# Optimization experiments

Hardware: AMD Instinct MI355X
Metric: run time of the kernel (lower is better)

The kernel has to match this reference:

```python
import jax, jax.numpy as jnp
import numpy as np
from jax import lax

FILTERS = [(1, 32), (2, 32), (3, 64), (4, 128), (5, 256), (6, 512), (7, 1024)]
CHAR_VOCAB, CHAR_DIM, MAX_CHARS = 262, 16, 50
N_FILTERS = sum(n for _, n in FILTERS)  # 2048
PROJ_DIM = 512
B, S = 16, 256


def setup_inputs() -> dict:
    key = jax.random.key(0)
    ks = jax.random.split(key, 32)
    inp = {}
    inp["words"] = jax.random.randint(ks[0], (B, S), 0, 50000)
    inp["chars"] = jax.random.randint(ks[1], (B, S, MAX_CHARS), 0, CHAR_VOCAB)
    inp["char_emb"] = jax.random.normal(ks[2], (CHAR_VOCAB, CHAR_DIM), jnp.float32) * 0.1
    for i, (w, n) in enumerate(FILTERS):
        inp[f"conv_w_{i}"] = jax.random.normal(ks[3 + i], (n, CHAR_DIM, w), jnp.float32) * 0.1
        inp[f"conv_b_{i}"] = jnp.zeros((n,), jnp.float32)
    for j in range(2):
        inp[f"hw_w_{j}"] = jax.random.normal(ks[12 + j], (2 * N_FILTERS, N_FILTERS), jnp.float32) * 0.02
        # Highway init: transform bias = 0, gate bias = 1
        inp[f"hw_b_{j}"] = jnp.concatenate([jnp.zeros((N_FILTERS,), jnp.float32), jnp.ones((N_FILTERS,), jnp.float32)])
    inp["proj_w"] = jax.random.normal(ks[20], (PROJ_DIM, N_FILTERS), jnp.float32) * 0.02
    inp["proj_b"] = jnp.zeros((PROJ_DIM,), jnp.float32)
    return inp


def _char_cnn(chars, char_emb, conv_ws, conv_bs, hw_ws, hw_bs, proj_w, proj_b):
    b, s, L = chars.shape
    # (B*S, CHAR_DIM, L)
    x = char_emb[chars].reshape(b * s, L, -1).transpose(0, 2, 1)
    convs = []
    for w, bias in zip(conv_ws, conv_bs):
        # Conv1d valid, NCW layout; y: (N, num, L-width+1)
        y = lax.conv_general_dilated(x, w, (1,), "VALID", dimension_numbers=("NCH", "OIH", "NCH"))
        y = y + bias[None, :, None]
        y = jnp.max(y, axis=-1)          # max over time
        convs.append(jax.nn.relu(y))      # activation
    h = jnp.concatenate(convs, axis=-1)   # (N, 2048)
    d = h.shape[-1]
    for W, bb in zip(hw_ws, hw_bs):
        p = h @ W.T + bb
        nonlinear = jax.nn.relu(p[:, :d])
        gate = jax.nn.sigmoid(p[:, d:])
        h = gate * h + (1.0 - gate) * nonlinear
    out = h @ proj_w.T + proj_b
    return out.reshape(b, s, -1)


def reference(words, chars, char_emb,
              conv_w_0, conv_b_0, conv_w_1, conv_b_1, conv_w_2, conv_b_2,
              conv_w_3, conv_b_3, conv_w_4, conv_b_4, conv_w_5, conv_b_5,
              conv_w_6, conv_b_6, hw_w_0, hw_b_0, hw_w_1, hw_b_1, proj_w, proj_b):
    conv_ws = [conv_w_0, conv_w_1, conv_w_2, conv_w_3, conv_w_4, conv_w_5, conv_w_6]
    conv_bs = [conv_b_0, conv_b_1, conv_b_2, conv_b_3, conv_b_4, conv_b_5, conv_b_6]
    return _char_cnn(chars, char_emb, conv_ws, conv_bs, [hw_w_0, hw_w_1], [hw_b_0, hw_b_1], proj_w, proj_b)
```

## Files before the change

### kernel.cpp

```cpp
#include <hip/hip_runtime.h>
#include <hip/hip_bf16.h>


#define NTOK 4096
#define NF   2048
#define KDIM 2048
#define HID  4096
#define PDIM 512

typedef __attribute__((ext_vector_type(4))) float floatx4;
typedef __attribute__((ext_vector_type(8))) short shortx8;

__device__ inline void async_copy16(const void* g, void* l) {
  __builtin_amdgcn_global_load_lds(
      (const __attribute__((address_space(1))) void*)(uintptr_t)g,
      (__attribute__((address_space(3))) void*)(uint32_t)(uintptr_t)l,
      16, 0, 0);
}

__global__ __launch_bounds__(256) void cvt_kernel(
    const float* __restrict__ s, __hip_bfloat16* __restrict__ d, int n) {
  int i = blockIdx.x * 256 + threadIdx.x;
  if (i < n) d[i] = __float2bfloat16(s[i]);
}

__global__ __launch_bounds__(256) void cvt_hw(
    const float* __restrict__ s, __hip_bfloat16* __restrict__ d) {
  int i = blockIdx.x * 256 + threadIdx.x;
  int r = i >> 11, k = i & 2047;
  int sr = (r >> 1) + (r & 1) * 2048;
  d[i] = __float2bfloat16(s[(size_t)sr * 2048 + k]);
}

__global__ __launch_bounds__(256) void conv_wprep(
    const float* __restrict__ w0, const float* __restrict__ w1,
    const float* __restrict__ w2, const float* __restrict__ w3,
    const float* __restrict__ w4, const float* __restrict__ w5,
    const float* __restrict__ w6,
    const float* __restrict__ b0, const float* __restrict__ b1,
    const float* __restrict__ b2, const float* __restrict__ b3,
    const float* __restrict__ b4, const float* __restrict__ b5,
    const float* __restrict__ b6, const float* __restrict__ emb,
    __hip_bfloat16* __restrict__ Wb, float* __restrict__ Bc,
    __hip_bfloat16* __restrict__ embb) {
  int idx = blockIdx.x * 256 + threadIdx.x;
  const int start[7] = {0, 32, 64, 128, 256, 512, 1024};
  const float* ws[7] = {w0, w1, w2, w3, w4, w5, w6};
  const float* bs[7] = {b0, b1, b2, b3, b4, b5, b6};
  if (idx < 262144) {
    int ch = idx >> 7, kp = idx & 127;
    int f = (ch >= 32) + (ch >= 64) + (ch >= 128) + (ch >= 256) +
            (ch >= 512) + (ch >= 1024);
    int w = f + 1, lc = ch - start[f];
    int d = kp & 15, k = kp >> 4;
    float v = (k < w) ? ws[f][((size_t)lc * 16 + d) * w + k] : 0.f;
    Wb[idx] = __float2bfloat16(v);
  } else if (idx < 262144 + 2048) {
    int ch = idx - 262144;
    int f = (ch >= 32) + (ch >= 64) + (ch >= 128) + (ch >= 256) +
            (ch >= 512) + (ch >= 1024);
    Bc[ch] = bs[f][ch - start[f]];
  } else if (idx < 262144 + 2048 + 4192) {
    int e = idx - 262144 - 2048;
    embb[e] = __float2bfloat16(emb[e]);
  }
}

template <int NKT, int NT, int ROWS>
__global__ __launch_bounds__(256) void conv_k(
    const int* __restrict__ chars, const __hip_bfloat16* __restrict__ embb,
    const __hip_bfloat16* __restrict__ Wb, const float* __restrict__ bias,
    __hip_bfloat16* __restrict__ h, int chbase) {
  __shared__ __align__(16) __hip_bfloat16 Xs[2 * 4 * ROWS * 24];
  int tid = threadIdx.x, wave = tid >> 6, lane = tid & 63;
  int frow = lane & 15, q = lane >> 4;
  int chb = chbase + blockIdx.y * 64;
  int tokbase = blockIdx.x * 32;

  shortx8 wreg[NKT][4];
#pragma unroll
  for (int kt = 0; kt < NKT; ++kt)
#pragma unroll
    for (int j = 0; j < 4; ++j)
      wreg[kt][j] = *(const shortx8*)(
          Wb + (size_t)(chb + j * 16 + frow) * 128 + kt * 32 + q * 8);

  float blane = bias[chb + lane];
  int Tvj[4];
#pragma unroll
  for (int j = 0; j < 4; ++j) {
    int ch = chb + j * 16 + frow;
    int w = 1 + (ch >= 32) + (ch >= 64) + (ch >= 128) + (ch >= 256) +
            (ch >= 512) + (ch >= 1024);
    Tvj[j] = 51 - w;
  }

  auto stage = [&](int g, int buf) {
    constexpr int NST = 4 * ROWS;
#pragma unroll
    for (int rep = 0; rep < (NST + 255) / 256; ++rep) {
      int rr = tid + rep * 256;
      if (rr < NST) {
        int tk = rr / ROWS, r = rr - tk * ROWS;
        __hip_bfloat16* dst = Xs + ((size_t)(buf * 4 + tk) * ROWS + r) * 24;
        if (r < 50) {
          int c = chars[(size_t)(tokbase + g * 4 + tk) * 50 + r];
          const shortx8* e = (const shortx8*)(embb + c * 16);
          *(shortx8*)(dst) = e[0];
          *(shortx8*)(dst + 8) = e[1];
        } else if (g <= 1) {
          shortx8 z = {0, 0, 0, 0, 0, 0, 0, 0};
          *(shortx8*)(dst) = z;
          *(shortx8*)(dst + 8) = z;
        }
      }
    }
  };

  stage(0, 0);
  __syncthreads();

  const floatx4 zero = {0.f, 0.f, 0.f, 0.f};
#pragma unroll 1
  for (int g = 0; g < 8; ++g) {
    if (g < 7) stage(g + 1, (g + 1) & 1);

    const __hip_bfloat16* Xw = Xs + (size_t)((g & 1) * 4 + wave) * ROWS * 24;
    floatx4 acc[NT][4];

#pragma unroll
    for (int kt = 0; kt < NKT; ++kt) {
      int kk = kt * 2 + (q >> 1);
      int d0 = (q & 1) * 8;
      shortx8 xf[NT];
#pragma unroll
      for (int i = 0; i < NT; ++i)
        xf[i] = *(const shortx8*)(Xw + (i * 16 + frow + kk) * 24 + d0);
#pragma unroll
      for (int i = 0; i < NT; ++i)
#pragma unroll
        for (int j = 0; j < 4; ++j) {
          if (kt == 0)
            acc[i][j] = __builtin_amdgcn_mfma_f32_16x16x32_bf16(
                xf[i], wreg[0][j], zero, 0, 0, 0);
          else
            acc[i][j] = __builtin_amdgcn_mfma_f32_16x16x32_bf16(
                xf[i], wreg[kt][j], acc[i][j], 0, 0, 0);
        }
    }

    float vj[4];
#pragma unroll
    for (int j = 0; j < 4; ++j) {
      float v = -1e30f;
#pragma unroll
      for (int i = 0; i < NT; ++i) {
#pragma unroll
        for (int r = 0; r < 4; ++r) {
          if (i < 2) {
            v = fmaxf(v, acc[i][j][r]);
          } else {
            int t = i * 16 + q * 4 + r;
            if (t < Tvj[j]) v = fmaxf(v, acc[i][j][r]);
          }
        }
      }
      v = fmaxf(v, __shfl_xor(v, 16));
      v = fmaxf(v, __shfl_xor(v, 32));
      vj[j] = v;
    }
    float r0 = (q & 2) ? vj[2] : vj[0];
    float r1 = (q & 2) ? vj[3] : vj[1];
    float rv = (q & 1) ? r1 : r0;
    int tok = tokbase + g * 4 + wave;
    h[(size_t)tok * NF + chb + lane] =
        __float2bfloat16(fmaxf(rv + blane, 0.f));
    __syncthreads();
  }
}

__global__ __launch_bounds__(256) void gemm_hw(
    const __hip_bfloat16* __restrict__ A, const __hip_bfloat16* __restrict__ B,
    const float* __restrict__ hwb, __hip_bfloat16* __restrict__ Hdst) {
  const int K = KDIM;
  __shared__ __align__(16) __hip_bfloat16 As[128 * 64];
  __shared__ __align__(16) __hip_bfloat16 Bs[128 * 64];
  int tid = threadIdx.x;
  int wave = tid >> 6, lane = tid & 63;
  int wr = wave >> 1, wc = wave & 1;
  int bn = blockIdx.y, bm = blockIdx.x;

  int sr8 = lane >> 3;
  int sc8 = lane & 7;
  int frow = lane & 15;
  int q    = lane >> 4;

  floatx4 acc[4][4];
  floatx4 zero = {0.f, 0.f, 0.f, 0.f};
#pragma unroll
  for (int i = 0; i < 4; ++i)
#pragma unroll
    for (int j = 0; j < 4; ++j) acc[i][j] = zero;

  const __hip_bfloat16* Ab = A + (size_t)bn * 128 * K;
  const __hip_bfloat16* Bb = B + (size_t)bm * 128 * K;

  for (int kb = 0; kb < K; kb += 64) {
    __syncthreads();
#pragma unroll
    for (int it = 0; it < 4; ++it) {
      int seg = wave * 4 + it;
      int r = seg * 8 + sr8;
      int gc = sc8 ^ (r & 7);
      async_copy16(Ab + (size_t)r * K + kb + gc * 8, (char*)As + seg * 1024);
      async_copy16(Bb + (size_t)r * K + kb + gc * 8, (char*)Bs + seg * 1024);
    }
    __syncthreads();

#pragma unroll
    for (int s = 0; s < 2; ++s) {
      shortx8 af[4], bf[4];
#pragma unroll
      for (int i = 0; i < 4; ++i) {
        int r = wr * 64 + i * 16 + frow;
        af[i] = *(const shortx8*)(As + r * 64 + ((s * 4 + q) ^ (r & 7)) * 8);
      }
#pragma unroll
      for (int j = 0; j < 4; ++j) {
        int r = wc * 64 + j * 16 + frow;
        bf[j] = *(const shortx8*)(Bs + r * 64 + ((s * 4 + q) ^ (r & 7)) * 8);
      }
#pragma unroll
      for (int i = 0; i < 4; ++i)
#pragma unroll
        for (int j = 0; j < 4; ++j)
          acc[i][j] = __builtin_amdgcn_mfma_f32_16x16x32_bf16(
              af[i], bf[j], acc[i][j], 0, 0, 0);
    }
  }

  int crow0 = bn * 128 + wr * 64 + q * 4;
  int ccol0 = bm * 128 + wc * 64 + frow;
#pragma unroll
  for (int i = 0; i < 4; ++i)
#pragma unroll
    for (int j = 0; j < 4; ++j) {
      int gcol = ccol0 + j * 16;
      float bb = (gcol & 1) ? hwb[2048 + (gcol >> 1)] : hwb[gcol >> 1];
#pragma unroll
      for (int r = 0; r < 4; ++r) {
        int row = crow0 + i * 16 + r;
        float v = acc[i][j][r] + bb;
        float partner = __shfl_xor(v, 1);
        if (!(lane & 1)) {
          float gte = 1.f / (1.f + expf(-partner));
          int ch = gcol >> 1;
          float hold = __bfloat162float(A[(size_t)row * 2048 + ch]);
          float hnew = gte * hold + (1.f - gte) * fmaxf(v, 0.f);
          Hdst[(size_t)row * 2048 + ch] = __float2bfloat16(hnew);
        }
      }
    }
}

__global__ __launch_bounds__(256) void gemm_proj(
    const __hip_bfloat16* __restrict__ A, const __hip_bfloat16* __restrict__ B,
    float* __restrict__ C, const float* __restrict__ bias) {
  const int K = KDIM;
  __shared__ __align__(16) __hip_bfloat16 As[32 * 64];
  __shared__ __align__(16) __hip_bfloat16 Bs[128 * 64];
  int tid = threadIdx.x;
  int wave = tid >> 6, lane = tid & 63;
  int wr = wave >> 1, wc = wave & 1;
  int bn = blockIdx.y, bm = blockIdx.x;

  int sr8 = lane >> 3, sc8 = lane & 7;
  int frow = lane & 15, q = lane >> 4;

  floatx4 acc[4];
  floatx4 zero = {0.f, 0.f, 0.f, 0.f};
#pragma unroll
  for (int j = 0; j < 4; ++j) acc[j] = zero;

  const __hip_bfloat16* Ab = A + (size_t)bn * 32 * K;
  const __hip_bfloat16* Bb = B + (size_t)bm * 128 * K;

  for (int kb = 0; kb < K; kb += 64) {
    __syncthreads();
    {
      int r = wave * 8 + sr8;
      int gc = sc8 ^ (r & 7);
      async_copy16(Ab + (size_t)r * K + kb + gc * 8, (char*)As + wave * 1024);
    }
#pragma unroll
    for (int it = 0; it < 4; ++it) {
      int seg = wave * 4 + it;
      int r = seg * 8 + sr8;
      int gc = sc8 ^ (r & 7);
      async_copy16(Bb + (size_t)r * K + kb + gc * 8, (char*)Bs + seg * 1024);
    }
    __syncthreads();

#pragma unroll
    for (int s = 0; s < 2; ++s) {
      shortx8 af, bf[4];
      {
        int r = wr * 16 + frow;
        af = *(const shortx8*)(As + r * 64 + ((s * 4 + q) ^ (r & 7)) * 8);
      }
#pragma unroll
      for (int j = 0; j < 4; ++j) {
        int r = wc * 64 + j * 16 + frow;
        bf[j] = *(const shortx8*)(Bs + r * 64 + ((s * 4 + q) ^ (r & 7)) * 8);
      }
#pragma unroll
      for (int j = 0; j < 4; ++j)
        acc[j] = __builtin_amdgcn_mfma_f32_16x16x32_bf16(af, bf[j], acc[j],
                                                          0, 0, 0);
    }
  }

  int crow0 = bn * 32 + wr * 16 + q * 4;
  int ccol0 = bm * 128 + wc * 64 + frow;
#pragma unroll
  for (int j = 0; j < 4; ++j) {
    int c = ccol0 + j * 16;
#pragma unroll
    for (int r = 0; r < 4; ++r) {
      int row = crow0 + r;
      C[(size_t)row * PDIM + c] = acc[j][r] + bias[c];
    }
  }
}

extern "C" void kernel_launch(void* const* d_in, const int* in_sizes, int n_in,
                              void* d_out, int out_size, void* d_ws, size_t ws_size,
                              hipStream_t stream) {
  const int*   chars  = (const int*)d_in[1];
  const float* emb    = (const float*)d_in[2];
  const float* cw[7];
  const float* cb[7];
  for (int i = 0; i < 7; ++i) {
    cw[i] = (const float*)d_in[3 + 2 * i];
    cb[i] = (const float*)d_in[4 + 2 * i];
  }
  const float* hw_w0  = (const float*)d_in[17];
  const float* hw_b0  = (const float*)d_in[18];
  const float* hw_w1  = (const float*)d_in[19];
  const float* hw_b1  = (const float*)d_in[20];
  const float* proj_w = (const float*)d_in[21];
  const float* proj_b = (const float*)d_in[22];
  float* out = (float*)d_out;

  char* ws = (char*)d_ws;
  __hip_bfloat16* h      = (__hip_bfloat16*)(ws);
  __hip_bfloat16* h2     = (__hip_bfloat16*)(ws + (16ull << 20));
  __hip_bfloat16* convWb = (__hip_bfloat16*)(ws + (32ull << 20));
  float*          convBc = (float*)(ws + (32ull << 20) + 524288);
  __hip_bfloat16* embb   = (__hip_bfloat16*)(ws + (32ull << 20) + 524288 + 8192);
  __hip_bfloat16* w0b    = (__hip_bfloat16*)(ws + (48ull << 20));
  __hip_bfloat16* w1b    = (__hip_bfloat16*)(ws + (64ull << 20));
  __hip_bfloat16* pwb    = (__hip_bfloat16*)(ws + (80ull << 20));

  cvt_hw<<<(HID * KDIM) / 256, 256, 0, stream>>>(hw_w0, w0b);
  cvt_hw<<<(HID * KDIM) / 256, 256, 0, stream>>>(hw_w1, w1b);
  cvt_kernel<<<(PDIM * KDIM) / 256, 256, 0, stream>>>(proj_w, pwb, PDIM * KDIM);
  conv_wprep<<<(262144 + 2048 + 4192 + 255) / 256, 256, 0, stream>>>(
      cw[0], cw[1], cw[2], cw[3], cw[4], cw[5], cw[6],
      cb[0], cb[1], cb[2], cb[3], cb[4], cb[5], cb[6], emb,
      convWb, convBc, embb);

  conv_k<1, 4, 72><<<dim3(128, 1), 256, 0, stream>>>(chars, embb, convWb,
                                                     convBc, h, 0);
  conv_k<2, 3, 56><<<dim3(128, 3), 256, 0, stream>>>(chars, embb, convWb,
                                                     convBc, h, 64);
  conv_k<3, 3, 56><<<dim3(128, 12), 256, 0, stream>>>(chars, embb, convWb,
                                                      convBc, h, 256);
  conv_k<4, 3, 56><<<dim3(128, 16), 256, 0, stream>>>(chars, embb, convWb,
                                                      convBc, h, 1024);

  gemm_hw<<<dim3(HID / 128, NTOK / 128), 256, 0, stream>>>(h, w0b, hw_b0, h2);
  gemm_hw<<<dim3(HID / 128, NTOK / 128), 256, 0, stream>>>(h2, w1b, hw_b1, h);
  gemm_proj<<<dim3(PDIM / 128, NTOK / 32), 256, 0, stream>>>(h, pwb, out,
                                                             proj_b);
}
```

Before: 520.4 us.

## Store GEMM LDS tiles in MFMA fragment order and split small conv launches

The highway and projection GEMMs now load global tiles into LDS already arranged in MFMA fragment order, so each lane reads a contiguous 16-byte slot at lane*16 with no XOR swizzle or per-load address math. The conv kernel gains a GROUPS template parameter, and the two smallest filter banks run with half as many token groups per block and twice as many blocks, to fill more CUs. Risks: the new LDS order may cause bank conflicts on reads or writes, and the global loads become less coalesced per row.

```diff
diff --git a/kernel.cpp b/kernel.cpp
--- a/kernel.cpp
+++ b/kernel.cpp
@@ -66,7 +66,7 @@
   }
 }
 
-template <int NKT, int NT, int ROWS>
+template <int NKT, int NT, int ROWS, int GROUPS>
 __global__ __launch_bounds__(256) void conv_k(
     const int* __restrict__ chars, const __hip_bfloat16* __restrict__ embb,
     const __hip_bfloat16* __restrict__ Wb, const float* __restrict__ bias,
@@ -75,7 +75,7 @@
   int tid = threadIdx.x, wave = tid >> 6, lane = tid & 63;
   int frow = lane & 15, q = lane >> 4;
   int chb = chbase + blockIdx.y * 64;
-  int tokbase = blockIdx.x * 32;
+  int tokbase = blockIdx.x * (GROUPS * 4);
 
   shortx8 wreg[NKT][4];
 #pragma unroll
@@ -122,8 +122,8 @@
 
   const floatx4 zero = {0.f, 0.f, 0.f, 0.f};
 #pragma unroll 1
-  for (int g = 0; g < 8; ++g) {
-    if (g < 7) stage(g + 1, (g + 1) & 1);
+  for (int g = 0; g < GROUPS; ++g) {
+    if (g < GROUPS - 1) stage(g + 1, (g + 1) & 1);
 
     const __hip_bfloat16* Xw = Xs + (size_t)((g & 1) * 4 + wave) * ROWS * 24;
     floatx4 acc[NT][4];
@@ -190,8 +190,6 @@
   int wr = wave >> 1, wc = wave & 1;
   int bn = blockIdx.y, bm = blockIdx.x;
 
-  int sr8 = lane >> 3;
-  int sc8 = lane & 7;
   int frow = lane & 15;
   int q    = lane >> 4;
 
@@ -204,16 +202,18 @@
 
   const __hip_bfloat16* Ab = A + (size_t)bn * 128 * K;
   const __hip_bfloat16* Bb = B + (size_t)bm * 128 * K;
+  const char* Ard = (const char*)As + lane * 16;
+  const char* Brd = (const char*)Bs + lane * 16;
 
   for (int kb = 0; kb < K; kb += 64) {
     __syncthreads();
 #pragma unroll
     for (int it = 0; it < 4; ++it) {
-      int seg = wave * 4 + it;
-      int r = seg * 8 + sr8;
-      int gc = sc8 ^ (r & 7);
-      async_copy16(Ab + (size_t)r * K + kb + gc * 8, (char*)As + seg * 1024);
-      async_copy16(Bb + (size_t)r * K + kb + gc * 8, (char*)Bs + seg * 1024);
+      int row = (wave * 2 + (it >> 1)) * 16 + frow;
+      int ck  = (it & 1) * 4 + q;
+      size_t src = (size_t)row * K + kb + ck * 8;
+      async_copy16(Ab + src, (char*)As + (wave * 4 + it) * 1024);
+      async_copy16(Bb + src, (char*)Bs + (wave * 4 + it) * 1024);
     }
     __syncthreads();
 
@@ -221,15 +221,11 @@
     for (int s = 0; s < 2; ++s) {
       shortx8 af[4], bf[4];
 #pragma unroll
-      for (int i = 0; i < 4; ++i) {
-        int r = wr * 64 + i * 16 + frow;
-        af[i] = *(const shortx8*)(As + r * 64 + ((s * 4 + q) ^ (r & 7)) * 8);
-      }
-#pragma unroll
-      for (int j = 0; j < 4; ++j) {
-        int r = wc * 64 + j * 16 + frow;
-        bf[j] = *(const shortx8*)(Bs + r * 64 + ((s * 4 + q) ^ (r & 7)) * 8);
-      }
+      for (int i = 0; i < 4; ++i)
+        af[i] = *(const shortx8*)(Ard + (wr * 4 + i) * 2048 + s * 1024);
+#pragma unroll
+      for (int j = 0; j < 4; ++j)
+        bf[j] = *(const shortx8*)(Brd + (wc * 4 + j) * 2048 + s * 1024);
 #pragma unroll
       for (int i = 0; i < 4; ++i)
 #pragma unroll
@@ -274,7 +270,6 @@
   int wr = wave >> 1, wc = wave & 1;
   int bn = blockIdx.y, bm = blockIdx.x;
 
-  int sr8 = lane >> 3, sc8 = lane & 7;
   int frow = lane & 15, q = lane >> 4;
 
   floatx4 acc[4];
@@ -284,35 +279,33 @@
 
   const __hip_bfloat16* Ab = A + (size_t)bn * 32 * K;
   const __hip_bfloat16* Bb = B + (size_t)bm * 128 * K;
+  const char* Ard = (const char*)As + lane * 16;
+  const char* Brd = (const char*)Bs + lane * 16;
 
   for (int kb = 0; kb < K; kb += 64) {
     __syncthreads();
     {
-      int r = wave * 8 + sr8;
-      int gc = sc8 ^ (r & 7);
-      async_copy16(Ab + (size_t)r * K + kb + gc * 8, (char*)As + wave * 1024);
+      int row = (wave >> 1) * 16 + frow;
+      int ck  = (wave & 1) * 4 + q;
+      async_copy16(Ab + (size_t)row * K + kb + ck * 8,
+                   (char*)As + wave * 1024);
     }
 #pragma unroll
     for (int it = 0; it < 4; ++it) {
-      int seg = wave * 4 + it;
-      int r = seg * 8 + sr8;
-      int gc = sc8 ^ (r & 7);
-      async_copy16(Bb + (size_t)r * K + kb + gc * 8, (char*)Bs + seg * 1024);
+      int row = (wave * 2 + (it >> 1)) * 16 + frow;
+      int ck  = (it & 1) * 4 + q;
+      async_copy16(Bb + (size_t)row * K + kb + ck * 8,
+                   (char*)Bs + (wave * 4 + it) * 1024);
     }
     __syncthreads();
 
 #pragma unroll
     for (int s = 0; s < 2; ++s) {
       shortx8 af, bf[4];
-      {
-        int r = wr * 16 + frow;
-        af = *(const shortx8*)(As + r * 64 + ((s * 4 + q) ^ (r & 7)) * 8);
-      }
-#pragma unroll
-      for (int j = 0; j < 4; ++j) {
-        int r = wc * 64 + j * 16 + frow;
-        bf[j] = *(const shortx8*)(Bs + r * 64 + ((s * 4 + q) ^ (r & 7)) * 8);
-      }
+      af = *(const shortx8*)(Ard + wr * 2048 + s * 1024);
+#pragma unroll
+      for (int j = 0; j < 4; ++j)
+        bf[j] = *(const shortx8*)(Brd + (wc * 4 + j) * 2048 + s * 1024);
 #pragma unroll
       for (int j = 0; j < 4; ++j)
         acc[j] = __builtin_amdgcn_mfma_f32_16x16x32_bf16(af, bf[j], acc[j],
@@ -370,14 +363,14 @@
       cb[0], cb[1], cb[2], cb[3], cb[4], cb[5], cb[6], emb,
       convWb, convBc, embb);
 
-  conv_k<1, 4, 72><<<dim3(128, 1), 256, 0, stream>>>(chars, embb, convWb,
-                                                     convBc, h, 0);
-  conv_k<2, 3, 56><<<dim3(128, 3), 256, 0, stream>>>(chars, embb, convWb,
-                                                     convBc, h, 64);
-  conv_k<3, 3, 56><<<dim3(128, 12), 256, 0, stream>>>(chars, embb, convWb,
-                                                      convBc, h, 256);
-  conv_k<4, 3, 56><<<dim3(128, 16), 256, 0, stream>>>(chars, embb, convWb,
-                                                      convBc, h, 1024);
+  conv_k<1, 4, 72, 4><<<dim3(256, 1), 256, 0, stream>>>(chars, embb, convWb,
+                                                        convBc, h, 0);
+  conv_k<2, 3, 56, 4><<<dim3(256, 3), 256, 0, stream>>>(chars, embb, convWb,
+                                                        convBc, h, 64);
+  conv_k<3, 3, 56, 8><<<dim3(128, 12), 256, 0, stream>>>(chars, embb, convWb,
+                                                         convBc, h, 256);
+  conv_k<4, 3, 56, 8><<<dim3(128, 16), 256, 0, stream>>>(chars, embb, convWb,
+                                                         convBc, h, 1024);
 
   gemm_hw<<<dim3(HID / 128, NTOK / 128), 256, 0, stream>>>(h, w0b, hw_b0, h2);
   gemm_hw<<<dim3(HID / 128, NTOK / 128), 256, 0, stream>>>(h2, w1b, hw_b1, h);
```

Measured after the change: 614.0 us. 1.18x slower.
